# Kernel tuning notes

Measured on AMD Instinct MI355X. Metric: run time of the kernel, lower is better.

Reference implementation:

```python
import jax, jax.numpy as jnp
import numpy as np

B, S, D, H = 2, 4096, 768, 12
DK = D // H


def setup_inputs() -> dict:
    key = jax.random.key(0)
    ks = jax.random.split(key, 12)
    inp = {
        "q": jax.random.normal(ks[0], (B, S, D), dtype=jnp.float32),
        "k": jax.random.normal(ks[1], (B, S, D), dtype=jnp.float32),
        "v": jax.random.normal(ks[2], (B, S, D), dtype=jnp.float32),
        "mask": jax.random.randint(ks[3], (B, 1, 1, S), 0, 2, dtype=jnp.int32),
        "w_q": jax.random.normal(ks[4], (D, D), dtype=jnp.float32) * 0.02,
        "b_q": jnp.zeros((D,), dtype=jnp.float32),
        "w_k": jax.random.normal(ks[5], (D, D), dtype=jnp.float32) * 0.02,
        "b_k": jnp.zeros((D,), dtype=jnp.float32),
        "w_v": jax.random.normal(ks[6], (D, D), dtype=jnp.float32) * 0.02,
        "b_v": jnp.zeros((D,), dtype=jnp.float32),
        "w_o": jax.random.normal(ks[7], (D, D), dtype=jnp.float32) * 0.02,
        "b_o": jnp.zeros((D,), dtype=jnp.float32),
    }
    return inp


def reference(q, k, v, mask, w_q, b_q, w_k, b_k, w_v, b_v, w_o, b_o):
    scale = 1.0 / jnp.sqrt(jnp.asarray(DK, dtype=q.dtype))
    # projections, then split heads: [B, S, H, DK]
    Q = (q @ w_q + b_q).reshape(B, S, H, DK)
    K = (k @ w_k + b_k).reshape(B, S, H, DK)
    V = (v @ w_v + b_v).reshape(B, S, H, DK)
    # scores: [B, H, Sq, Sk]
    scores = jnp.einsum("bqhd,bkhd->bhqk", Q, K) * scale
    scores = jnp.where(mask == 0, jnp.asarray(-1e9, dtype=scores.dtype), scores)
    attn = jax.nn.softmax(scores, axis=-1)
    # dropout prob is 0.0 (eval): identity
    out = jnp.einsum("bhqk,bkhd->bqhd", attn, V).reshape(B, S, D)
    return out @ w_o + b_o
```

## Files before the change

### kernel.cpp

```cpp
#include <hip/hip_runtime.h>
#include <hip/hip_bf16.h>
#include <stdint.h>

typedef __bf16 bf16;
typedef bf16 bf16x8 __attribute__((ext_vector_type(8)));
typedef float f32x4 __attribute__((ext_vector_type(4)));

constexpr int CB  = 2;
constexpr int CS  = 4096;
constexpr int CD  = 768;
constexpr int CH  = 12;
constexpr int CDK = 64;
constexpr int CBH = CB * CH;
constexpr int CM  = CB * CS;

__device__ __forceinline__ void gload16(const void* g, void* l) {
  __builtin_amdgcn_global_load_lds((const __attribute__((address_space(1))) void*)g,
                                   (__attribute__((address_space(3))) void*)l, 16, 0, 0);
}

__device__ __forceinline__ float fast_exp2(float x) {
#if __has_builtin(__builtin_amdgcn_exp2f)
  return __builtin_amdgcn_exp2f(x);
#else
  return exp2f(x);
#endif
}

__device__ __forceinline__ uint32_t cvtpk_bf16(float lo, float hi) {
  uint32_t r;
  asm("v_cvt_pk_bf16_f32 %0, %1, %2" : "=v"(r) : "v"(lo), "v"(hi));
  return r;
}

__global__ __launch_bounds__(256) void k_convert3(const float* __restrict__ q, const float* __restrict__ k,
                                                  const float* __restrict__ v,
                                                  bf16* __restrict__ qo, bf16* __restrict__ ko,
                                                  bf16* __restrict__ vo, int n8) {
  const float* in; bf16* out;
  if      (blockIdx.y == 0) { in = q; out = qo; }
  else if (blockIdx.y == 1) { in = k; out = ko; }
  else                      { in = v; out = vo; }
  int i = blockIdx.x * 256 + threadIdx.x;
  if (i >= n8) return;
  const float4* p = (const float4*)in;
  float4 a = p[i * 2], b = p[i * 2 + 1];
  bf16x8 o;
  o[0] = (bf16)a.x; o[1] = (bf16)a.y; o[2] = (bf16)a.z; o[3] = (bf16)a.w;
  o[4] = (bf16)b.x; o[5] = (bf16)b.y; o[6] = (bf16)b.z; o[7] = (bf16)b.w;
  ((bf16x8*)out)[i] = o;
}

__global__ __launch_bounds__(256) void k_wtrans(const float* __restrict__ w0, const float* __restrict__ w1,
                                                const float* __restrict__ w2, const float* __restrict__ w3,
                                                bf16* __restrict__ o0, bf16* __restrict__ o1,
                                                bf16* __restrict__ o2, bf16* __restrict__ o3) {
  const float* w; bf16* o;
  if      (blockIdx.z == 0) { w = w0; o = o0; }
  else if (blockIdx.z == 1) { w = w1; o = o1; }
  else if (blockIdx.z == 2) { w = w2; o = o2; }
  else                      { w = w3; o = o3; }
  __shared__ float t[32][33];
  int k0 = blockIdx.x * 32, n0 = blockIdx.y * 32;
  int tx = threadIdx.x & 31, ty = threadIdx.x >> 5;
#pragma unroll
  for (int i = 0; i < 4; ++i) {
    int kk = ty + i * 8;
    t[kk][tx] = w[(size_t)(k0 + kk) * CD + n0 + tx];
  }
  __syncthreads();
#pragma unroll
  for (int i = 0; i < 4; ++i) {
    int nn = ty + i * 8;
    o[(size_t)(n0 + nn) * CD + k0 + tx] = (bf16)t[tx][nn];
  }
}

template <int EPI>
__device__ __forceinline__ void gemm_core(const bf16* __restrict__ A, const bf16* __restrict__ Bt,
                                          const float* __restrict__ bias, void* __restrict__ outp,
                                          int K, int mtile, int ntile) {
  __shared__ bf16 As[2][128 * 32];
  __shared__ bf16 Bs[2][128 * 32];
  const int tid = threadIdx.x;
  const int lane = tid & 63;
  const int wid = tid >> 6;
  const int wr = wid >> 1, wc = wid & 1;
  const int r = lane & 15, g = lane >> 4;
  const int m0 = mtile * 128, n0 = ntile * 128;

  f32x4 acc[4][4] = {};

  auto stageAB = [&](int bsel, int kt) {
#pragma unroll
    for (int i = 0; i < 2; ++i) {
      int flat = tid * 8 + i * 2048;
      int rr = flat >> 5, cc = flat & 31;
      gload16(A + (size_t)(m0 + rr) * K + kt + cc, (char*)&As[bsel][0] + (size_t)flat * 2);
    }
#pragma unroll
    for (int i = 0; i < 2; ++i) {
      int flat = tid * 8 + i * 2048;
      int rr = flat >> 5, cc = flat & 31;
      gload16(Bt + (size_t)(n0 + rr) * K + kt + cc, (char*)&Bs[bsel][0] + (size_t)flat * 2);
    }
  };

  stageAB(0, 0);
  const int NKT = K / 32;
  for (int t = 0; t < NKT; ++t) {
    __syncthreads();
    if (t + 1 < NKT) stageAB((t + 1) & 1, (t + 1) * 32);
    const bf16* Asb = &As[t & 1][0];
    const bf16* Bsb = &Bs[t & 1][0];

    bf16x8 af[4], bfr[4];
#pragma unroll
    for (int mi = 0; mi < 4; ++mi)
      af[mi] = *(const bf16x8*)(Asb + (wr * 64 + mi * 16 + r) * 32 + g * 8);
#pragma unroll
    for (int ni = 0; ni < 4; ++ni)
      bfr[ni] = *(const bf16x8*)(Bsb + (wc * 64 + ni * 16 + r) * 32 + g * 8);
    __builtin_amdgcn_s_setprio(1);
#pragma unroll
    for (int mi = 0; mi < 4; ++mi)
#pragma unroll
      for (int ni = 0; ni < 4; ++ni)
        acc[mi][ni] = __builtin_amdgcn_mfma_f32_16x16x32_bf16(af[mi], bfr[ni], acc[mi][ni], 0, 0, 0);
    __builtin_amdgcn_s_setprio(0);
  }

  if (EPI == 0) {
    bf16* o = (bf16*)outp;
#pragma unroll
    for (int ni = 0; ni < 4; ++ni) {
      int col = n0 + wc * 64 + ni * 16 + r;
      float bv = bias[col];
      int h = col >> 6, dk = col & 63;
#pragma unroll
      for (int mi = 0; mi < 4; ++mi) {
#pragma unroll
        for (int q = 0; q < 4; ++q) {
          int row = m0 + wr * 64 + mi * 16 + g * 4 + q;
          int b = row >> 12, s = row & 4095;
          o[(size_t)((b * CH + h) * CS + s) * CDK + dk] = (bf16)(acc[mi][ni][q] + bv);
        }
      }
    }
  } else {
    float* o = (float*)outp;
#pragma unroll
    for (int ni = 0; ni < 4; ++ni) {
      int col = n0 + wc * 64 + ni * 16 + r;
      float bv = bias[col];
#pragma unroll
      for (int mi = 0; mi < 4; ++mi) {
#pragma unroll
        for (int q = 0; q < 4; ++q) {
          int row = m0 + wr * 64 + mi * 16 + g * 4 + q;
          o[(size_t)row * CD + col] = acc[mi][ni][q] + bv;
        }
      }
    }
  }
}

__global__ __launch_bounds__(256) void k_qkv(const bf16* __restrict__ qb, const bf16* __restrict__ kb,
                                             const bf16* __restrict__ vb,
                                             const bf16* __restrict__ wqT, const bf16* __restrict__ wkT,
                                             const bf16* __restrict__ wvT,
                                             const float* __restrict__ bq, const float* __restrict__ bk,
                                             const float* __restrict__ bv,
                                             bf16* __restrict__ Qh, bf16* __restrict__ Kh,
                                             bf16* __restrict__ Vh) {
  const bf16* A; const bf16* W; const float* bias; bf16* O;
  if      (blockIdx.z == 0) { A = qb; W = wqT; bias = bq; O = Qh; }
  else if (blockIdx.z == 1) { A = kb; W = wkT; bias = bk; O = Kh; }
  else                      { A = vb; W = wvT; bias = bv; O = Vh; }
  gemm_core<0>(A, W, bias, O, CD, blockIdx.x, blockIdx.y);
}

__global__ __launch_bounds__(256) void k_out(const bf16* __restrict__ ao, const bf16* __restrict__ woT,
                                             const float* __restrict__ bo, float* __restrict__ out) {
  gemm_core<1>(ao, woT, bo, out, CD, blockIdx.x, blockIdx.y);
}

__global__ __launch_bounds__(256) void k_scan(const int* __restrict__ mask, int* __restrict__ idx,
                                              int* __restrict__ nk) {
  int b = blockIdx.x;
  const int* m = mask + b * CS;
  int tid = threadIdx.x, lane = tid & 63, wv = tid >> 6;
  int base = tid * 16;
  int mv[16];
  const int4* m4 = (const int4*)(m + base);
#pragma unroll
  for (int i = 0; i < 4; ++i) {
    int4 x = m4[i];
    mv[i * 4 + 0] = x.x; mv[i * 4 + 1] = x.y; mv[i * 4 + 2] = x.z; mv[i * 4 + 3] = x.w;
  }
  int local = 0;
#pragma unroll
  for (int j = 0; j < 16; ++j) local += (mv[j] != 0);
  int pre = local;
#pragma unroll
  for (int d = 1; d < 64; d <<= 1) {
    int t = __shfl_up(pre, d, 64);
    if (lane >= d) pre += t;
  }
  __shared__ int wsum[4];
  if (lane == 63) wsum[wv] = pre;
  __syncthreads();
  int woff = 0;
  for (int w = 0; w < wv; ++w) woff += wsum[w];
  int pos = woff + pre - local;
  int* ib = idx + b * CS;
#pragma unroll
  for (int j = 0; j < 16; ++j)
    if (mv[j]) ib[pos++] = base + j;
  if (tid == 255) nk[b] = woff + pre;
}

__global__ __launch_bounds__(256) void k_gather(const bf16* __restrict__ Kh, const bf16* __restrict__ Vh,
                                                const int* __restrict__ idx, const int* __restrict__ nk,
                                                bf16* __restrict__ Kc, bf16* __restrict__ VTc) {
  int bh = blockIdx.y, b = bh / CH;
  int nkb = nk[b];
  int nkp = (nkb + 63) & ~63;
  int i0 = blockIdx.x * 64;
  if (i0 >= nkp) return;
  const int* ib = idx + b * CS;
  int tid = threadIdx.x;
  __shared__ bf16 t[64][72];
#pragma unroll
  for (int i = 0; i < 2; ++i) {
    int f = tid + i * 256;
    int ii = f >> 3, c8 = (f & 7) << 3;
    int gi = i0 + ii;
    bf16x8 kv = {}, vv = {};
    if (gi < nkb) {
      int s = ib[gi];
      kv = *(const bf16x8*)&Kh[((size_t)bh * CS + s) * CDK + c8];
      vv = *(const bf16x8*)&Vh[((size_t)bh * CS + s) * CDK + c8];
    }
    *(bf16x8*)&Kc[((size_t)bh * CS + gi) * CDK + c8] = kv;
#pragma unroll
    for (int j = 0; j < 8; ++j) t[ii][c8 + j] = vv[j];
  }
  __syncthreads();
#pragma unroll
  for (int i = 0; i < 2; ++i) {
    int f = tid + i * 256;
    int d = f >> 3, s8 = (f & 7) << 3;
    bf16x8 vv;
#pragma unroll
    for (int j = 0; j < 8; ++j) vv[j] = t[s8 + j][d];
    *(bf16x8*)&VTc[((size_t)bh * CDK + d) * CS + i0 + s8] = vv;
  }
}

__device__ __forceinline__ int KSWZ(int key) { return ((key & 3) + ((key >> 3) & 1) * 4) << 4; }

__global__ __launch_bounds__(256) void k_attn(const bf16* __restrict__ Qh, const bf16* __restrict__ Kc,
                                              const bf16* __restrict__ VTc, const int* __restrict__ nk,
                                              bf16* __restrict__ attn_out) {
  __shared__ bf16 Ks[2][64 * 64];
  __shared__ bf16 VTs[2][64 * 64];

  const int tid = threadIdx.x;
  const int lane = tid & 63, wv = tid >> 6;
  const int r = lane & 15, g = lane >> 4;
  const int bh = blockIdx.y;
  const int b = bh / CH, h = bh % CH;
  const int q0 = blockIdx.x * 128 + wv * 32;
  const int nkb = nk[b];
  const int ntiles = (nkb + 63) >> 6;

  bf16x8 aq[2][2];
#pragma unroll
  for (int rg = 0; rg < 2; ++rg) {
    size_t qrow = (size_t)bh * CS + q0 + rg * 16 + r;
    aq[rg][0] = *(const bf16x8*)&Qh[qrow * CDK + g * 8];
    aq[rg][1] = *(const bf16x8*)&Qh[qrow * CDK + 32 + g * 8];
  }

  f32x4 accO[2][4] = {};
  float m_run[2] = {0.f, 0.f}, l_run[2] = {0.f, 0.f};

  const float cs = 0.18033688f;

  auto stage = [&](int bsel, int kt) {
    char* KsB0 = (char*)&Ks[bsel][0];
    char* VTsB0 = (char*)&VTs[bsel][0];
#pragma unroll
    for (int i = 0; i < 2; ++i) {
      int f = tid + i * 256;
      int row = f >> 3, sl = f & 7;
      int srcb = (sl * 16) ^ KSWZ(row);
      gload16(Kc + (size_t)(bh * CS + kt + row) * CDK + (srcb >> 1), KsB0 + (size_t)f * 16);
    }
#pragma unroll
    for (int i = 0; i < 2; ++i) {
      int f = tid + i * 256;
      int row = f >> 3, sl = f & 7;
      int srcb = (sl * 16) ^ ((row & 7) << 4);
      gload16(VTc + (size_t)(bh * CDK + row) * CS + kt + (srcb >> 1), VTsB0 + (size_t)f * 16);
    }
  };

  stage(0, 0);

  for (int t = 0; t < ntiles; ++t) {
    __syncthreads();
    if (t + 1 < ntiles) stage((t + 1) & 1, (t + 1) * 64);
    const int kt = t * 64;
    char* KsB = (char*)&Ks[t & 1][0];
    char* VTsB = (char*)&VTs[t & 1][0];
    const bool tail = (kt + 64 > nkb);

#pragma unroll
    for (int rg = 0; rg < 2; ++rg) {
      float p[16];
      __builtin_amdgcn_s_setprio(1);
#pragma unroll
      for (int kb = 0; kb < 4; ++kb) {
        const int key = 8 * (r >> 2) + 32 * (kb >> 1) + 4 * (kb & 1) + (r & 3);
        f32x4 s = {};
#pragma unroll
        for (int kh = 0; kh < 2; ++kh) {
          int byteoff = key * 128 + ((kh * 64 + g * 16) ^ KSWZ(key));
          bf16x8 ka = *(const bf16x8*)(KsB + byteoff);
          s = __builtin_amdgcn_mfma_f32_16x16x32_bf16(ka, aq[rg][kh], s, 0, 0, 0);
        }
#pragma unroll
        for (int q = 0; q < 4; ++q) p[kb * 4 + q] = s[q] * cs;
      }
      __builtin_amdgcn_s_setprio(0);
      if (tail) {
#pragma unroll
        for (int kb = 0; kb < 4; ++kb)
#pragma unroll
          for (int q = 0; q < 4; ++q)
            if (kt + 8 * g + 32 * (kb >> 1) + 4 * (kb & 1) + q >= nkb) p[kb * 4 + q] = -1e30f;
      }

      float pm = p[0];
#pragma unroll
      for (int j = 1; j < 16; ++j) pm = fmaxf(pm, p[j]);
      pm = fmaxf(pm, __shfl_xor(pm, 16, 64));
      pm = fmaxf(pm, __shfl_xor(pm, 32, 64));

      if (__any(pm > m_run[rg] + 8.f)) {
        float mnew = fmaxf(m_run[rg], pm);
        float corr = fast_exp2(m_run[rg] - mnew);
        m_run[rg] = mnew;
        l_run[rg] *= corr;
#pragma unroll
        for (int q = 0; q < 4; ++q) {
          float cq = __shfl(corr, 20 * g + q, 64);
#pragma unroll
          for (int nb = 0; nb < 4; ++nb) accO[rg][nb][q] *= cq;
        }
      }

      float rsum = 0.f;
      union { uint32_t u[8]; bf16x8 v[2]; } pk;
#pragma unroll
      for (int kb = 0; kb < 4; ++kb) {
        float e0 = fast_exp2(p[kb * 4 + 0] - m_run[rg]);
        float e1 = fast_exp2(p[kb * 4 + 1] - m_run[rg]);
        float e2 = fast_exp2(p[kb * 4 + 2] - m_run[rg]);
        float e3 = fast_exp2(p[kb * 4 + 3] - m_run[rg]);
        rsum += (e0 + e1) + (e2 + e3);
        pk.u[kb * 2 + 0] = cvtpk_bf16(e0, e1);
        pk.u[kb * 2 + 1] = cvtpk_bf16(e2, e3);
      }
      rsum += __shfl_xor(rsum, 16, 64);
      rsum += __shfl_xor(rsum, 32, 64);
      l_run[rg] += rsum;

      __builtin_amdgcn_s_setprio(1);
#pragma unroll
      for (int nb = 0; nb < 4; ++nb) {
#pragma unroll
        for (int kh = 0; kh < 2; ++kh) {
          int d = nb * 16 + r;
          int byteoff = d * 128 + ((kh * 64 + g * 16) ^ ((d & 7) << 4));
          bf16x8 bvf = *(const bf16x8*)(VTsB + byteoff);
          accO[rg][nb] = __builtin_amdgcn_mfma_f32_16x16x32_bf16(pk.v[kh], bvf, accO[rg][nb], 0, 0, 0);
        }
      }
      __builtin_amdgcn_s_setprio(0);
    }
  }

#pragma unroll
  for (int rg = 0; rg < 2; ++rg) {
#pragma unroll
    for (int q = 0; q < 4; ++q) {
      float lq = __shfl(l_run[rg], 20 * g + q, 64);
      float inv = 1.f / lq;
      int srow = q0 + rg * 16 + g * 4 + q;
      size_t bs = (size_t)b * CS + srow;
#pragma unroll
      for (int nb = 0; nb < 4; ++nb) {
        int d = nb * 16 + r;
        attn_out[bs * CD + h * 64 + d] = (bf16)(accO[rg][nb][q] * inv);
      }
    }
  }
}

extern "C" void kernel_launch(void* const* d_in, const int* in_sizes, int n_in,
                              void* d_out, int out_size, void* d_ws, size_t ws_size,
                              hipStream_t stream) {
  const float* q   = (const float*)d_in[0];
  const float* k   = (const float*)d_in[1];
  const float* v   = (const float*)d_in[2];
  const int*  mask = (const int*)d_in[3];
  const float* w_q = (const float*)d_in[4];
  const float* b_q = (const float*)d_in[5];
  const float* w_k = (const float*)d_in[6];
  const float* b_k = (const float*)d_in[7];
  const float* w_v = (const float*)d_in[8];
  const float* b_v = (const float*)d_in[9];
  const float* w_o = (const float*)d_in[10];
  const float* b_o = (const float*)d_in[11];

  char* ws = (char*)d_ws;
  size_t off = 0;
  auto alloc = [&](size_t bytes) { char* p = ws + off; off += (bytes + 255) & ~255ULL; return p; };

  const size_t MD2 = (size_t)CM * CD * 2;
  const size_t WT2 = (size_t)CD * CD * 2;
  bf16* qb  = (bf16*)alloc(MD2);
  bf16* kb  = (bf16*)alloc(MD2);
  bf16* vb  = (bf16*)alloc(MD2);
  bf16* wqT = (bf16*)alloc(WT2);
  bf16* wkT = (bf16*)alloc(WT2);
  bf16* wvT = (bf16*)alloc(WT2);
  bf16* woT = (bf16*)alloc(WT2);
  bf16* Qh  = (bf16*)alloc(MD2);
  bf16* Kh  = (bf16*)alloc(MD2);
  bf16* Vh  = (bf16*)alloc(MD2);
  int*  idx = (int*)alloc((size_t)CB * CS * 4);
  int*  nkd = (int*)alloc(256);
  bf16* Kc  = qb;
  bf16* VTc = kb;
  bf16* ao  = vb;
  (void)ws_size; (void)in_sizes; (void)n_in; (void)out_size;

  const int n8 = CM * CD / 8;
  dim3 blk(256);

  k_convert3<<<dim3((n8 + 255) / 256, 3), blk, 0, stream>>>(q, k, v, qb, kb, vb, n8);
  k_wtrans<<<dim3(CD / 32, CD / 32, 4), blk, 0, stream>>>(w_q, w_k, w_v, w_o, wqT, wkT, wvT, woT);
  k_scan<<<dim3(CB), blk, 0, stream>>>(mask, idx, nkd);
  k_qkv<<<dim3(CM / 128, CD / 128, 3), blk, 0, stream>>>(qb, kb, vb, wqT, wkT, wvT, b_q, b_k, b_v, Qh, Kh, Vh);
  k_gather<<<dim3(CS / 64, CBH), blk, 0, stream>>>(Kh, Vh, idx, nkd, Kc, VTc);
  k_attn<<<dim3(CS / 128, CBH), blk, 0, stream>>>(Qh, Kc, VTc, nkd, ao);
  k_out<<<dim3(CM / 128, CD / 128), blk, 0, stream>>>(ao, woT, b_o, (float*)d_out);
}
```

Baseline: 186.0 us.

## Switch pipeline to fp16, fold softmax scale into Wq, use packed fp16 exp and MFMA row sums

Converts all intermediate tensors and MFMAs from bf16 to fp16 and folds the softmax scale (with log2e) into the Q projection weights and bias, which removes the per-score multiply. In the attention kernel, scores are packed to fp16 early so max and exp2 run on packed half2 values, and row sums come from an extra MFMA against a ones vector rather than scalar adds and shuffles. This targets VALU work in the softmax inner loop. The cost is reduced exponent range and precision in fp16 for scores and exponentials.

```diff
diff --git a/kernel.cpp b/kernel.cpp
--- a/kernel.cpp
+++ b/kernel.cpp
@@ -1,9 +1,10 @@
 #include <hip/hip_runtime.h>
-#include <hip/hip_bf16.h>
+#include <hip/hip_fp16.h>
 #include <stdint.h>
 
-typedef __bf16 bf16;
-typedef bf16 bf16x8 __attribute__((ext_vector_type(8)));
+typedef _Float16 hf;
+typedef hf hfx8 __attribute__((ext_vector_type(8)));
+typedef hf hfx2 __attribute__((ext_vector_type(2)));
 typedef float f32x4 __attribute__((ext_vector_type(4)));
 
 constexpr int CB  = 2;
@@ -13,6 +14,7 @@
 constexpr int CDK = 64;
 constexpr int CBH = CB * CH;
 constexpr int CM  = CB * CS;
+constexpr float CS_SCALE = 0.18033688f;
 
 __device__ __forceinline__ void gload16(const void* g, void* l) {
   __builtin_amdgcn_global_load_lds((const __attribute__((address_space(1))) void*)g,
@@ -27,17 +29,11 @@
 #endif
 }
 
-__device__ __forceinline__ uint32_t cvtpk_bf16(float lo, float hi) {
-  uint32_t r;
-  asm("v_cvt_pk_bf16_f32 %0, %1, %2" : "=v"(r) : "v"(lo), "v"(hi));
-  return r;
-}
-
 __global__ __launch_bounds__(256) void k_convert3(const float* __restrict__ q, const float* __restrict__ k,
                                                   const float* __restrict__ v,
-                                                  bf16* __restrict__ qo, bf16* __restrict__ ko,
-                                                  bf16* __restrict__ vo, int n8) {
-  const float* in; bf16* out;
+                                                  hf* __restrict__ qo, hf* __restrict__ ko,
+                                                  hf* __restrict__ vo, int n8) {
+  const float* in; hf* out;
   if      (blockIdx.y == 0) { in = q; out = qo; }
   else if (blockIdx.y == 1) { in = k; out = ko; }
   else                      { in = v; out = vo; }
@@ -45,18 +41,19 @@
   if (i >= n8) return;
   const float4* p = (const float4*)in;
   float4 a = p[i * 2], b = p[i * 2 + 1];
-  bf16x8 o;
-  o[0] = (bf16)a.x; o[1] = (bf16)a.y; o[2] = (bf16)a.z; o[3] = (bf16)a.w;
-  o[4] = (bf16)b.x; o[5] = (bf16)b.y; o[6] = (bf16)b.z; o[7] = (bf16)b.w;
-  ((bf16x8*)out)[i] = o;
+  hfx8 o;
+  o[0] = (hf)a.x; o[1] = (hf)a.y; o[2] = (hf)a.z; o[3] = (hf)a.w;
+  o[4] = (hf)b.x; o[5] = (hf)b.y; o[6] = (hf)b.z; o[7] = (hf)b.w;
+  ((hfx8*)out)[i] = o;
 }
 
 __global__ __launch_bounds__(256) void k_wtrans(const float* __restrict__ w0, const float* __restrict__ w1,
                                                 const float* __restrict__ w2, const float* __restrict__ w3,
-                                                bf16* __restrict__ o0, bf16* __restrict__ o1,
-                                                bf16* __restrict__ o2, bf16* __restrict__ o3) {
-  const float* w; bf16* o;
-  if      (blockIdx.z == 0) { w = w0; o = o0; }
+                                                hf* __restrict__ o0, hf* __restrict__ o1,
+                                                hf* __restrict__ o2, hf* __restrict__ o3) {
+  const float* w; hf* o;
+  float sc = 1.f;
+  if      (blockIdx.z == 0) { w = w0; o = o0; sc = CS_SCALE; }
   else if (blockIdx.z == 1) { w = w1; o = o1; }
   else if (blockIdx.z == 2) { w = w2; o = o2; }
   else                      { w = w3; o = o3; }
@@ -72,16 +69,17 @@
 #pragma unroll
   for (int i = 0; i < 4; ++i) {
     int nn = ty + i * 8;
-    o[(size_t)(n0 + nn) * CD + k0 + tx] = (bf16)t[tx][nn];
+    o[(size_t)(n0 + nn) * CD + k0 + tx] = (hf)(t[tx][nn] * sc);
   }
 }
 
 template <int EPI>
-__device__ __forceinline__ void gemm_core(const bf16* __restrict__ A, const bf16* __restrict__ Bt,
-                                          const float* __restrict__ bias, void* __restrict__ outp,
+__device__ __forceinline__ void gemm_core(const hf* __restrict__ A, const hf* __restrict__ Bt,
+                                          const float* __restrict__ bias, float bsc,
+                                          void* __restrict__ outp,
                                           int K, int mtile, int ntile) {
-  __shared__ bf16 As[2][128 * 32];
-  __shared__ bf16 Bs[2][128 * 32];
+  __shared__ hf As[2][128 * 32];
+  __shared__ hf Bs[2][128 * 32];
   const int tid = threadIdx.x;
   const int lane = tid & 63;
   const int wid = tid >> 6;
@@ -111,48 +109,48 @@
   for (int t = 0; t < NKT; ++t) {
     __syncthreads();
     if (t + 1 < NKT) stageAB((t + 1) & 1, (t + 1) * 32);
-    const bf16* Asb = &As[t & 1][0];
-    const bf16* Bsb = &Bs[t & 1][0];
-
-    bf16x8 af[4], bfr[4];
+    const hf* Asb = &As[t & 1][0];
+    const hf* Bsb = &Bs[t & 1][0];
+
+    hfx8 af[4], bfr[4];
 #pragma unroll
     for (int mi = 0; mi < 4; ++mi)
-      af[mi] = *(const bf16x8*)(Asb + (wr * 64 + mi * 16 + r) * 32 + g * 8);
+      af[mi] = *(const hfx8*)(Asb + (wr * 64 + mi * 16 + r) * 32 + g * 8);
 #pragma unroll
     for (int ni = 0; ni < 4; ++ni)
-      bfr[ni] = *(const bf16x8*)(Bsb + (wc * 64 + ni * 16 + r) * 32 + g * 8);
+      bfr[ni] = *(const hfx8*)(Bsb + (wc * 64 + ni * 16 + r) * 32 + g * 8);
     __builtin_amdgcn_s_setprio(1);
 #pragma unroll
     for (int mi = 0; mi < 4; ++mi)
 #pragma unroll
       for (int ni = 0; ni < 4; ++ni)
-        acc[mi][ni] = __builtin_amdgcn_mfma_f32_16x16x32_bf16(af[mi], bfr[ni], acc[mi][ni], 0, 0, 0);
+        acc[mi][ni] = __builtin_amdgcn_mfma_f32_16x16x32_f16(af[mi], bfr[ni], acc[mi][ni], 0, 0, 0);
     __builtin_amdgcn_s_setprio(0);
   }
 
   if (EPI == 0) {
-    bf16* o = (bf16*)outp;
+    hf* o = (hf*)outp;
+#pragma unroll
+    for (int ni = 0; ni < 4; ++ni) {
+      int col = n0 + wc * 64 + ni * 16 + r;
+      float bv = bias[col] * bsc;
+      int h = col >> 6, dk = col & 63;
+#pragma unroll
+      for (int mi = 0; mi < 4; ++mi) {
+#pragma unroll
+        for (int q = 0; q < 4; ++q) {
+          int row = m0 + wr * 64 + mi * 16 + g * 4 + q;
+          int b = row >> 12, s = row & 4095;
+          o[(size_t)((b * CH + h) * CS + s) * CDK + dk] = (hf)(acc[mi][ni][q] + bv);
+        }
+      }
+    }
+  } else {
+    float* o = (float*)outp;
 #pragma unroll
     for (int ni = 0; ni < 4; ++ni) {
       int col = n0 + wc * 64 + ni * 16 + r;
       float bv = bias[col];
-      int h = col >> 6, dk = col & 63;
-#pragma unroll
-      for (int mi = 0; mi < 4; ++mi) {
-#pragma unroll
-        for (int q = 0; q < 4; ++q) {
-          int row = m0 + wr * 64 + mi * 16 + g * 4 + q;
-          int b = row >> 12, s = row & 4095;
-          o[(size_t)((b * CH + h) * CS + s) * CDK + dk] = (bf16)(acc[mi][ni][q] + bv);
-        }
-      }
-    }
-  } else {
-    float* o = (float*)outp;
-#pragma unroll
-    for (int ni = 0; ni < 4; ++ni) {
-      int col = n0 + wc * 64 + ni * 16 + r;
-      float bv = bias[col];
 #pragma unroll
       for (int mi = 0; mi < 4; ++mi) {
 #pragma unroll
@@ -165,24 +163,24 @@
   }
 }
 
-__global__ __launch_bounds__(256) void k_qkv(const bf16* __restrict__ qb, const bf16* __restrict__ kb,
-                                             const bf16* __restrict__ vb,
-                                             const bf16* __restrict__ wqT, const bf16* __restrict__ wkT,
-                                             const bf16* __restrict__ wvT,
+__global__ __launch_bounds__(256) void k_qkv(const hf* __restrict__ qb, const hf* __restrict__ kb,
+                                             const hf* __restrict__ vb,
+                                             const hf* __restrict__ wqT, const hf* __restrict__ wkT,
+                                             const hf* __restrict__ wvT,
                                              const float* __restrict__ bq, const float* __restrict__ bk,
                                              const float* __restrict__ bv,
-                                             bf16* __restrict__ Qh, bf16* __restrict__ Kh,
-                                             bf16* __restrict__ Vh) {
-  const bf16* A; const bf16* W; const float* bias; bf16* O;
-  if      (blockIdx.z == 0) { A = qb; W = wqT; bias = bq; O = Qh; }
+                                             hf* __restrict__ Qh, hf* __restrict__ Kh,
+                                             hf* __restrict__ Vh) {
+  const hf* A; const hf* W; const float* bias; hf* O; float bsc = 1.f;
+  if      (blockIdx.z == 0) { A = qb; W = wqT; bias = bq; O = Qh; bsc = CS_SCALE; }
   else if (blockIdx.z == 1) { A = kb; W = wkT; bias = bk; O = Kh; }
   else                      { A = vb; W = wvT; bias = bv; O = Vh; }
-  gemm_core<0>(A, W, bias, O, CD, blockIdx.x, blockIdx.y);
-}
-
-__global__ __launch_bounds__(256) void k_out(const bf16* __restrict__ ao, const bf16* __restrict__ woT,
+  gemm_core<0>(A, W, bias, bsc, O, CD, blockIdx.x, blockIdx.y);
+}
+
+__global__ __launch_bounds__(256) void k_out(const hf* __restrict__ ao, const hf* __restrict__ woT,
                                              const float* __restrict__ bo, float* __restrict__ out) {
-  gemm_core<1>(ao, woT, bo, out, CD, blockIdx.x, blockIdx.y);
+  gemm_core<1>(ao, woT, bo, 1.f, out, CD, blockIdx.x, blockIdx.y);
 }
 
 __global__ __launch_bounds__(256) void k_scan(const int* __restrict__ mask, int* __restrict__ idx,
@@ -220,9 +218,9 @@
   if (tid == 255) nk[b] = woff + pre;
 }
 
-__global__ __launch_bounds__(256) void k_gather(const bf16* __restrict__ Kh, const bf16* __restrict__ Vh,
+__global__ __launch_bounds__(256) void k_gather(const hf* __restrict__ Kh, const hf* __restrict__ Vh,
                                                 const int* __restrict__ idx, const int* __restrict__ nk,
-                                                bf16* __restrict__ Kc, bf16* __restrict__ VTc) {
+                                                hf* __restrict__ Kc, hf* __restrict__ VTc) {
   int bh = blockIdx.y, b = bh / CH;
   int nkb = nk[b];
   int nkp = (nkb + 63) & ~63;
@@ -230,19 +228,19 @@
   if (i0 >= nkp) return;
   const int* ib = idx + b * CS;
   int tid = threadIdx.x;
-  __shared__ bf16 t[64][72];
+  __shared__ hf t[64][72];
 #pragma unroll
   for (int i = 0; i < 2; ++i) {
     int f = tid + i * 256;
     int ii = f >> 3, c8 = (f & 7) << 3;
     int gi = i0 + ii;
-    bf16x8 kv = {}, vv = {};
+    hfx8 kv = {}, vv = {};
     if (gi < nkb) {
       int s = ib[gi];
-      kv = *(const bf16x8*)&Kh[((size_t)bh * CS + s) * CDK + c8];
-      vv = *(const bf16x8*)&Vh[((size_t)bh * CS + s) * CDK + c8];
-    }
-    *(bf16x8*)&Kc[((size_t)bh * CS + gi) * CDK + c8] = kv;
+      kv = *(const hfx8*)&Kh[((size_t)bh * CS + s) * CDK + c8];
+      vv = *(const hfx8*)&Vh[((size_t)bh * CS + s) * CDK + c8];
+    }
+    *(hfx8*)&Kc[((size_t)bh * CS + gi) * CDK + c8] = kv;
 #pragma unroll
     for (int j = 0; j < 8; ++j) t[ii][c8 + j] = vv[j];
   }
@@ -251,20 +249,20 @@
   for (int i = 0; i < 2; ++i) {
     int f = tid + i * 256;
     int d = f >> 3, s8 = (f & 7) << 3;
-    bf16x8 vv;
+    hfx8 vv;
 #pragma unroll
     for (int j = 0; j < 8; ++j) vv[j] = t[s8 + j][d];
-    *(bf16x8*)&VTc[((size_t)bh * CDK + d) * CS + i0 + s8] = vv;
+    *(hfx8*)&VTc[((size_t)bh * CDK + d) * CS + i0 + s8] = vv;
   }
 }
 
 __device__ __forceinline__ int KSWZ(int key) { return ((key & 3) + ((key >> 3) & 1) * 4) << 4; }
 
-__global__ __launch_bounds__(256) void k_attn(const bf16* __restrict__ Qh, const bf16* __restrict__ Kc,
-                                              const bf16* __restrict__ VTc, const int* __restrict__ nk,
-                                              bf16* __restrict__ attn_out) {
-  __shared__ bf16 Ks[2][64 * 64];
-  __shared__ bf16 VTs[2][64 * 64];
+__global__ __launch_bounds__(256) void k_attn(const hf* __restrict__ Qh, const hf* __restrict__ Kc,
+                                              const hf* __restrict__ VTc, const int* __restrict__ nk,
+                                              hf* __restrict__ attn_out) {
+  __shared__ hf Ks[2][64 * 64];
+  __shared__ hf VTs[2][64 * 64];
 
   const int tid = threadIdx.x;
   const int lane = tid & 63, wv = tid >> 6;
@@ -275,18 +273,21 @@
   const int nkb = nk[b];
   const int ntiles = (nkb + 63) >> 6;
 
-  bf16x8 aq[2][2];
+  hfx8 aq[2][2];
 #pragma unroll
   for (int rg = 0; rg < 2; ++rg) {
     size_t qrow = (size_t)bh * CS + q0 + rg * 16 + r;
-    aq[rg][0] = *(const bf16x8*)&Qh[qrow * CDK + g * 8];
-    aq[rg][1] = *(const bf16x8*)&Qh[qrow * CDK + 32 + g * 8];
-  }
+    aq[rg][0] = *(const hfx8*)&Qh[qrow * CDK + g * 8];
+    aq[rg][1] = *(const hfx8*)&Qh[qrow * CDK + 32 + g * 8];
+  }
+
+  hfx8 ones;
+#pragma unroll
+  for (int j = 0; j < 8; ++j) ones[j] = (hf)1.f;
 
   f32x4 accO[2][4] = {};
-  float m_run[2] = {0.f, 0.f}, l_run[2] = {0.f, 0.f};
-
-  const float cs = 0.18033688f;
+  f32x4 l_acc[2] = {};
+  float m_run[2] = {0.f, 0.f};
 
   auto stage = [&](int bsel, int kt) {
     char* KsB0 = (char*)&Ks[bsel][0];
@@ -319,7 +320,7 @@
 
 #pragma unroll
     for (int rg = 0; rg < 2; ++rg) {
-      float p[16];
+      hfx2 hp[8];
       __builtin_amdgcn_s_setprio(1);
 #pragma unroll
       for (int kb = 0; kb < 4; ++kb) {
@@ -328,24 +329,25 @@
 #pragma unroll
         for (int kh = 0; kh < 2; ++kh) {
           int byteoff = key * 128 + ((kh * 64 + g * 16) ^ KSWZ(key));
-          bf16x8 ka = *(const bf16x8*)(KsB + byteoff);
-          s = __builtin_amdgcn_mfma_f32_16x16x32_bf16(ka, aq[rg][kh], s, 0, 0, 0);
-        }
-#pragma unroll
-        for (int q = 0; q < 4; ++q) p[kb * 4 + q] = s[q] * cs;
+          hfx8 ka = *(const hfx8*)(KsB + byteoff);
+          s = __builtin_amdgcn_mfma_f32_16x16x32_f16(ka, aq[rg][kh], s, 0, 0, 0);
+        }
+        if (tail) {
+#pragma unroll
+          for (int q = 0; q < 4; ++q)
+            if (kt + 8 * g + 32 * (kb >> 1) + 4 * (kb & 1) + q >= nkb) s[q] = -1024.f;
+        }
+        hp[kb * 2 + 0] = __builtin_bit_cast(hfx2, __builtin_amdgcn_cvt_pkrtz(s[0], s[1]));
+        hp[kb * 2 + 1] = __builtin_bit_cast(hfx2, __builtin_amdgcn_cvt_pkrtz(s[2], s[3]));
       }
       __builtin_amdgcn_s_setprio(0);
-      if (tail) {
-#pragma unroll
-        for (int kb = 0; kb < 4; ++kb)
-#pragma unroll
-          for (int q = 0; q < 4; ++q)
-            if (kt + 8 * g + 32 * (kb >> 1) + 4 * (kb & 1) + q >= nkb) p[kb * 4 + q] = -1e30f;
-      }
-
-      float pm = p[0];
-#pragma unroll
-      for (int j = 1; j < 16; ++j) pm = fmaxf(pm, p[j]);
+
+      hfx2 hm = __builtin_elementwise_max(
+          __builtin_elementwise_max(__builtin_elementwise_max(hp[0], hp[1]),
+                                    __builtin_elementwise_max(hp[2], hp[3])),
+          __builtin_elementwise_max(__builtin_elementwise_max(hp[4], hp[5]),
+                                    __builtin_elementwise_max(hp[6], hp[7])));
+      float pm = fmaxf((float)hm[0], (float)hm[1]);
       pm = fmaxf(pm, __shfl_xor(pm, 16, 64));
       pm = fmaxf(pm, __shfl_xor(pm, 32, 64));
 
@@ -353,40 +355,34 @@
         float mnew = fmaxf(m_run[rg], pm);
         float corr = fast_exp2(m_run[rg] - mnew);
         m_run[rg] = mnew;
-        l_run[rg] *= corr;
 #pragma unroll
         for (int q = 0; q < 4; ++q) {
           float cq = __shfl(corr, 20 * g + q, 64);
 #pragma unroll
           for (int nb = 0; nb < 4; ++nb) accO[rg][nb][q] *= cq;
-        }
-      }
-
-      float rsum = 0.f;
-      union { uint32_t u[8]; bf16x8 v[2]; } pk;
-#pragma unroll
-      for (int kb = 0; kb < 4; ++kb) {
-        float e0 = fast_exp2(p[kb * 4 + 0] - m_run[rg]);
-        float e1 = fast_exp2(p[kb * 4 + 1] - m_run[rg]);
-        float e2 = fast_exp2(p[kb * 4 + 2] - m_run[rg]);
-        float e3 = fast_exp2(p[kb * 4 + 3] - m_run[rg]);
-        rsum += (e0 + e1) + (e2 + e3);
-        pk.u[kb * 2 + 0] = cvtpk_bf16(e0, e1);
-        pk.u[kb * 2 + 1] = cvtpk_bf16(e2, e3);
-      }
-      rsum += __shfl_xor(rsum, 16, 64);
-      rsum += __shfl_xor(rsum, 32, 64);
-      l_run[rg] += rsum;
+          l_acc[rg][q] *= cq;
+        }
+      }
+
+      union { hfx2 h2[8]; hfx8 v[2]; } pk;
+      const hf mh = (hf)m_run[rg];
+      const hfx2 mh2 = {mh, mh};
+#pragma unroll
+      for (int j = 0; j < 8; ++j)
+        pk.h2[j] = __builtin_elementwise_exp2(hp[j] - mh2);
 
       __builtin_amdgcn_s_setprio(1);
+#pragma unroll
+      for (int kh = 0; kh < 2; ++kh)
+        l_acc[rg] = __builtin_amdgcn_mfma_f32_16x16x32_f16(pk.v[kh], ones, l_acc[rg], 0, 0, 0);
 #pragma unroll
       for (int nb = 0; nb < 4; ++nb) {
 #pragma unroll
         for (int kh = 0; kh < 2; ++kh) {
           int d = nb * 16 + r;
           int byteoff = d * 128 + ((kh * 64 + g * 16) ^ ((d & 7) << 4));
-          bf16x8 bvf = *(const bf16x8*)(VTsB + byteoff);
-          accO[rg][nb] = __builtin_amdgcn_mfma_f32_16x16x32_bf16(pk.v[kh], bvf, accO[rg][nb], 0, 0, 0);
+          hfx8 bvf = *(const hfx8*)(VTsB + byteoff);
+          accO[rg][nb] = __builtin_amdgcn_mfma_f32_16x16x32_f16(pk.v[kh], bvf, accO[rg][nb], 0, 0, 0);
         }
       }
       __builtin_amdgcn_s_setprio(0);
@@ -397,14 +393,13 @@
   for (int rg = 0; rg < 2; ++rg) {
 #pragma unroll
     for (int q = 0; q < 4; ++q) {
-      float lq = __shfl(l_run[rg], 20 * g + q, 64);
-      float inv = 1.f / lq;
+      float inv = 1.f / l_acc[rg][q];
       int srow = q0 + rg * 16 + g * 4 + q;
       size_t bs = (size_t)b * CS + srow;
 #pragma unroll
       for (int nb = 0; nb < 4; ++nb) {
         int d = nb * 16 + r;
-        attn_out[bs * CD + h * 64 + d] = (bf16)(accO[rg][nb][q] * inv);
+        attn_out[bs * CD + h * 64 + d] = (hf)(accO[rg][nb][q] * inv);
       }
     }
   }
@@ -432,21 +427,21 @@
 
   const size_t MD2 = (size_t)CM * CD * 2;
   const size_t WT2 = (size_t)CD * CD * 2;
-  bf16* qb  = (bf16*)alloc(MD2);
-  bf16* kb  = (bf16*)alloc(MD2);
-  bf16* vb  = (bf16*)alloc(MD2);
-  bf16* wqT = (bf16*)alloc(WT2);
-  bf16* wkT = (bf16*)alloc(WT2);
-  bf16* wvT = (bf16*)alloc(WT2);
-  bf16* woT = (bf16*)alloc(WT2);
-  bf16* Qh  = (bf16*)alloc(MD2);
-  bf16* Kh  = (bf16*)alloc(MD2);
-  bf16* Vh  = (bf16*)alloc(MD2);
-  int*  idx = (int*)alloc((size_t)CB * CS * 4);
-  int*  nkd = (int*)alloc(256);
-  bf16* Kc  = qb;
-  bf16* VTc = kb;
-  bf16* ao  = vb;
+  hf* qb  = (hf*)alloc(MD2);
+  hf* kb  = (hf*)alloc(MD2);
+  hf* vb  = (hf*)alloc(MD2);
+  hf* wqT = (hf*)alloc(WT2);
+  hf* wkT = (hf*)alloc(WT2);
+  hf* wvT = (hf*)alloc(WT2);
+  hf* woT = (hf*)alloc(WT2);
+  hf* Qh  = (hf*)alloc(MD2);
+  hf* Kh  = (hf*)alloc(MD2);
+  hf* Vh  = (hf*)alloc(MD2);
+  int* idx = (int*)alloc((size_t)CB * CS * 4);
+  int* nkd = (int*)alloc(256);
+  hf* Kc  = qb;
+  hf* VTc = kb;
+  hf* ao  = vb;
   (void)ws_size; (void)in_sizes; (void)n_in; (void)out_size;
 
   const int n8 = CM * CD / 8;
```

New measurement: 181.9 us. -2.2%, faster.
